# Kernel optimization log

Hardware: AMD Instinct MI355X
Metric: run time of the kernel (lower is better)

Reference implementation:

```python
import jax, jax.numpy as jnp
import numpy as np

V = 50257   # vocab_size
E = 512     # word_vec_size
H = 512     # hidden_size
L = 2       # num_layers
SOS = 1     # sos_id


def setup_inputs() -> dict:
    key = jax.random.key(0)
    ks = jax.random.split(key, 14)
    B, T, S = 32, 32, 128
    return {
        'tgt_seqs': jax.random.randint(ks[0], (B, T), 0, V),
        'decoder_hidden': jax.random.normal(ks[1], (L, B, H), jnp.float32) * 0.1,
        'encoder_outputs': jax.random.normal(ks[2], (S, B, H), jnp.float32),
        'attention_mask': jnp.zeros((B, S), dtype=bool),  # True = masked position
        'emb_W': jax.random.normal(ks[3], (V, E), jnp.float32) * 0.02,
        'gru_Wih': jax.random.normal(ks[4], (L, 3 * H, E), jnp.float32) * 0.02,
        'gru_Whh': jax.random.normal(ks[5], (L, 3 * H, H), jnp.float32) * 0.02,
        'gru_bih': jnp.zeros((L, 3 * H), jnp.float32),
        'gru_bhh': jnp.zeros((L, 3 * H), jnp.float32),
        'Wa': jax.random.normal(ks[6], (H, H), jnp.float32) * 0.02,
        'ba': jnp.zeros((H,), jnp.float32),
        'Wc': jax.random.normal(ks[7], (H, 2 * H), jnp.float32) * 0.02,
        'bc': jnp.zeros((H,), jnp.float32),
        'Ws': jax.random.normal(ks[8], (V, H), jnp.float32) * 0.02,
        'bs': jnp.zeros((V,), jnp.float32),
    }


def reference(tgt_seqs, decoder_hidden, encoder_outputs, attention_mask,
              emb_W, gru_Wih, gru_Whh, gru_bih, gru_bhh,
              Wa, ba, Wc, bc, Ws, bs):
    B, T = tgt_seqs.shape
    Hh = decoder_hidden.shape[-1]
    enc = jnp.transpose(encoder_outputs, (1, 0, 2))            # (B, S, H)
    enc_proj = jnp.einsum('bsh,gh->bsg', enc, Wa) + ba         # W_a(enc), precomputed
    # teacher-forced inputs: sos then shifted targets, time-major (T, B)
    tokens = jnp.concatenate(
        [jnp.full((B, 1), SOS, tgt_seqs.dtype), tgt_seqs[:, :-1]], axis=1).T

    def step(h, tok):
        x = emb_W[tok]                                          # (B, E)
        hs = []
        for l in range(L):                                      # small fixed layer loop
            gx = x @ gru_Wih[l].T + gru_bih[l]
            gh = h[l] @ gru_Whh[l].T + gru_bhh[l]
            r = jax.nn.sigmoid(gx[:, :Hh] + gh[:, :Hh])
            z = jax.nn.sigmoid(gx[:, Hh:2 * Hh] + gh[:, Hh:2 * Hh])
            n = jnp.tanh(gx[:, 2 * Hh:] + r * gh[:, 2 * Hh:])
            x = (1.0 - z) * n + z * h[l]
            hs.append(x)
        h_new = jnp.stack(hs)                                   # (L, B, H)
        # Luong general attention
        scores = jnp.einsum('bh,bsh->bs', x, enc_proj)          # (B, S)
        scores = jnp.where(attention_mask, -1e9, scores)
        attn = jax.nn.softmax(scores, axis=-1)
        ctx = jnp.einsum('bs,bsh->bh', attn, enc)               # (B, H)
        concat = jnp.tanh(jnp.concatenate([ctx, x], axis=-1) @ Wc.T + bc)
        return h_new, concat

    h_final, concats = jax.lax.scan(step, decoder_hidden, tokens)  # concats: (T, B, H)
    decoder_outputs = jnp.einsum('tbh,vh->tbv', concats, Ws) + bs  # (T, B, V)
    return decoder_outputs, h_final
```

## Files before the change

### kernel.cpp

```cpp
#include <hip/hip_runtime.h>
#include <hip/hip_bf16.h>
#include <stdint.h>
#include <stddef.h>

#define B_ 32
#define T_ 32
#define S_ 128
#define H_ 512
#define V_ 50257
#define VPAD 50304
#define TH3 1536

typedef __attribute__((ext_vector_type(8))) short short8x;
typedef __attribute__((ext_vector_type(4))) float f32x4;

__device__ __forceinline__ float sigf(float x) { return 1.f / (1.f + __expf(-x)); }
__device__ __forceinline__ float tanhfast(float x) {
  float e = __expf(2.f * x);
  return 1.f - 2.f / (e + 1.f);
}
__device__ __forceinline__ unsigned short f2bf(float x) {
  unsigned int u = __float_as_uint(x);
  return (unsigned short)((u + 0x7fffu + ((u >> 16) & 1u)) >> 16);
}
__device__ __forceinline__ float dot4(float4 a, float4 b) {
  return a.x * b.x + a.y * b.y + a.z * b.z + a.w * b.w;
}

__device__ __forceinline__ void async16(const unsigned short* g, short* l) {
  __builtin_amdgcn_global_load_lds(
      (const __attribute__((address_space(1))) unsigned int*)g,
      (__attribute__((address_space(3))) unsigned int*)l, 16, 0, 0);
}

__device__ __forceinline__ void store_wt(float* p, float v) {
  asm volatile("global_store_dword %0, %1, off sc0 sc1" :: "v"(p), "v"(v) : "memory");
}
__device__ __forceinline__ void store_wt4(float* p, f32x4 v) {
  asm volatile("global_store_dwordx4 %0, %1, off sc0 sc1" :: "v"(p), "v"(v) : "memory");
}

__device__ __forceinline__ void wait_flags(const int* flags, int n) {
  if (threadIdx.x < 64) {
    const int j = threadIdx.x;
    bool d0 = (j >= n), d1 = (j + 64 >= n);
    while (true) {
      if (!d0) d0 = __hip_atomic_load(flags + (size_t)j * 32, __ATOMIC_RELAXED,
                                      __HIP_MEMORY_SCOPE_SYSTEM) != 0;
      if (!d1) d1 = __hip_atomic_load(flags + (size_t)(j + 64) * 32, __ATOMIC_RELAXED,
                                      __HIP_MEMORY_SCOPE_SYSTEM) != 0;
      if (__all(d0 && d1)) break;
      __builtin_amdgcn_s_sleep(4);
    }
  }
  __syncthreads();
}

__device__ __forceinline__ void drain_and_flag(int* flag) {
  asm volatile("s_waitcnt vmcnt(0)" ::: "memory");
  __syncthreads();
  if (threadIdx.x == 0)
    __hip_atomic_store(flag, 1, __ATOMIC_RELAXED, __HIP_MEMORY_SCOPE_SYSTEM);
}

__global__ __launch_bounds__(256) void cvt_kernel(const float* __restrict__ Ws,
                                                  unsigned short* __restrict__ outb) {
  size_t i = ((size_t)blockIdx.x * 256 + threadIdx.x) * 4;
  if (i >= (size_t)VPAD * 512) return;
  float4 f;
  if (i < (size_t)V_ * 512) f = *(const float4*)(Ws + i);
  else f = make_float4(0.f, 0.f, 0.f, 0.f);
  ushort4 u;
  u.x = f2bf(f.x); u.y = f2bf(f.y); u.z = f2bf(f.z); u.w = f2bf(f.w);
  *(ushort4*)(outb + i) = u;
}

template <int MODE>
__global__ __launch_bounds__(256) void gemm_f32(const float* __restrict__ Asrc,
                                                const float* __restrict__ Bw,
                                                const float* __restrict__ bias,
                                                float* __restrict__ Cout,
                                                const int* __restrict__ tgt, int N) {
  __shared__ __align__(16) float As[16][68];
  __shared__ __align__(16) float Bs[16][68];
  const int tid = threadIdx.x;
  const int tx = tid & 15, ty = tid >> 4;
  const int m0 = blockIdx.y * 64, n0 = blockIdx.x * 64;
  const int srow = tid >> 2, skq = (tid & 3) * 4;
  const float* arow;
  {
    int m = m0 + srow;
    if (MODE == 0) {
      int t = m >> 5, b = m & 31;
      int tok = (t == 0) ? 1 : tgt[b * 32 + t - 1];
      arow = Asrc + (size_t)tok * 512;
    } else {
      int b = m >> 7, s = m & 127;
      arow = Asrc + ((size_t)s * 32 + b) * 512;
    }
  }
  const float* brow = Bw + (size_t)(n0 + srow) * 512;
  float acc[4][4] = {};
  for (int k0 = 0; k0 < 512; k0 += 16) {
    float4 av = *(const float4*)(arow + k0 + skq);
    float4 bv = *(const float4*)(brow + k0 + skq);
    __syncthreads();
    As[skq + 0][srow] = av.x; As[skq + 1][srow] = av.y;
    As[skq + 2][srow] = av.z; As[skq + 3][srow] = av.w;
    Bs[skq + 0][srow] = bv.x; Bs[skq + 1][srow] = bv.y;
    Bs[skq + 2][srow] = bv.z; Bs[skq + 3][srow] = bv.w;
    __syncthreads();
#pragma unroll
    for (int kk = 0; kk < 16; ++kk) {
      float4 a4 = *(const float4*)&As[kk][ty * 4];
      float4 b4 = *(const float4*)&Bs[kk][tx * 4];
      acc[0][0] += a4.x * b4.x; acc[0][1] += a4.x * b4.y; acc[0][2] += a4.x * b4.z; acc[0][3] += a4.x * b4.w;
      acc[1][0] += a4.y * b4.x; acc[1][1] += a4.y * b4.y; acc[1][2] += a4.y * b4.z; acc[1][3] += a4.y * b4.w;
      acc[2][0] += a4.z * b4.x; acc[2][1] += a4.z * b4.y; acc[2][2] += a4.z * b4.z; acc[2][3] += a4.z * b4.w;
      acc[3][0] += a4.w * b4.x; acc[3][1] += a4.w * b4.y; acc[3][2] += a4.w * b4.z; acc[3][3] += a4.w * b4.w;
    }
  }
  float4 b4 = *(const float4*)(bias + n0 + tx * 4);
#pragma unroll
  for (int i = 0; i < 4; ++i) {
    float4 o;
    o.x = acc[i][0] + b4.x; o.y = acc[i][1] + b4.y;
    o.z = acc[i][2] + b4.z; o.w = acc[i][3] + b4.w;
    *(float4*)(Cout + (size_t)(m0 + ty * 4 + i) * N + n0 + tx * 4) = o;
  }
}

__device__ __forceinline__ void cat_rows(int t, int gg, int b2, const float* wr,
                                         const float* __restrict__ ctxbuf,
                                         const float* __restrict__ x1buf,
                                         const float* __restrict__ bc,
                                         unsigned short* __restrict__ cbf) {
  const float* ctx = ctxbuf + (size_t)t * 16384 + b2 * 512;
  const float* x1c = x1buf + (size_t)t * 16384 + b2 * 512;
  float a = bc[gg];
#pragma unroll 4
  for (int k = 0; k < 512; k += 4) a += dot4(*(const float4*)(wr + k), *(const float4*)(ctx + k));
#pragma unroll 4
  for (int k = 0; k < 512; k += 4) a += dot4(*(const float4*)(wr + 512 + k), *(const float4*)(x1c + k));
  cbf[((size_t)t * 32 + b2) * 512 + gg] = f2bf(tanhfast(a));
}

__global__ __launch_bounds__(256) void seq_kernel(
    const float* __restrict__ dh, const float* __restrict__ enc,
    const unsigned char* __restrict__ mask,
    const float* __restrict__ Whh, const float* __restrict__ Wih,
    const float* __restrict__ bih, const float* __restrict__ bhh,
    const float* __restrict__ Wc, const float* __restrict__ bc,
    const float* __restrict__ gx0v, const float* __restrict__ encp,
    int* __restrict__ bar, float* __restrict__ x0buf, float* __restrict__ x1buf,
    float* __restrict__ attnbuf, float* __restrict__ ctxbuf,
    unsigned short* __restrict__ cbf, float* __restrict__ out_hf) {
  const int tid = threadIdx.x, bid = blockIdx.x;
  __shared__ __align__(16) float sm[3456];
  __shared__ __align__(16) float wlds[12288];
  const int lane = tid & 63, wv = tid >> 6;
  const int bb = lane & 31, rh = lane >> 5;

  int* fx0 = bar;
  int* fx1 = bar + 65536;
  int* fattn = bar + 196608;
  int* fctx = bar + 229376;

  if (bid < 64) {
    const int iset0 = bid * 8;
    for (int idx = tid; idx < 24 * 128; idx += 256) {
      const int rloc = idx >> 7, kq = (idx & 127) << 2;
      const int g = rloc >> 3, ii = rloc & 7;
      *(float4*)&wlds[rloc * 512 + kq] =
          *(const float4*)(Whh + (size_t)(g * 512 + iset0 + ii) * 512 + kq);
    }
  } else if (bid < 192) {
    const int iset0 = (bid - 64) * 4;
    for (int idx = tid; idx < 12 * 128; idx += 256) {
      const int rloc = idx >> 7, kq = (idx & 127) << 2;
      const int g = rloc >> 2, ii = rloc & 3;
      const size_t off = (size_t)(1536 + g * 512 + iset0 + ii) * 512 + kq;
      *(float4*)&wlds[rloc * 512 + kq] = *(const float4*)(Wih + off);
      *(float4*)&wlds[(12 + rloc) * 512 + kq] = *(const float4*)(Whh + off);
    }
  } else {
    const int gg0 = (bid < 224) ? (bid - 192) * 8 : 256 + (bid - 224) * 8;
    for (int idx = tid; idx < 8 * 256; idx += 256) {
      const int r = idx >> 8, kq = (idx & 255) << 2;
      *(float4*)&wlds[r * 1024 + kq] =
          *(const float4*)(Wc + (size_t)(gg0 + r) * 1024 + kq);
    }
  }
  __syncthreads();

  if (bid < 64) {
    const int iset0 = bid * 8;
    for (int t = 0; t < 32; ++t) {
      if (t > 0) wait_flags(fx0 + (size_t)(t - 1) * 2048, 64);
      const float* xsrc = (t == 0) ? dh : (x0buf + (size_t)(t - 1) * 16384);
      float acc[12];
#pragma unroll
      for (int r = 0; r < 12; ++r) acc[r] = 0.f;
      const float* xb = xsrc + bb * 512 + wv * 128;
      for (int c = 0; c < 4; ++c) {
        float4 xv[8];
#pragma unroll
        for (int u = 0; u < 8; ++u) xv[u] = *(const float4*)(xb + c * 32 + u * 4);
#pragma unroll
        for (int rr = 0; rr < 12; ++rr) {
          const int rloc = rh * 12 + rr;
          const float* wrow = wlds + (size_t)rloc * 512 + wv * 128 + c * 32;
#pragma unroll
          for (int u = 0; u < 8; ++u)
            acc[rr] += dot4(*(const float4*)(wrow + u * 4), xv[u]);
        }
      }
      __syncthreads();
#pragma unroll
      for (int rr = 0; rr < 12; ++rr)
        sm[wv * 768 + (rh * 12 + rr) * 32 + bb] = acc[rr];
      __syncthreads();
      {
        const int b2 = tid & 31, i2 = tid >> 5;
        const int ig = iset0 + i2;
        float s0 = bhh[ig], s1 = bhh[512 + ig], s2 = bhh[1024 + ig];
#pragma unroll
        for (int w = 0; w < 4; ++w) {
          s0 += sm[w * 768 + (i2) * 32 + b2];
          s1 += sm[w * 768 + (8 + i2) * 32 + b2];
          s2 += sm[w * 768 + (16 + i2) * 32 + b2];
        }
        const float* gx = gx0v + ((size_t)t * 32 + b2) * 1536;
        const float hv = xsrc[b2 * 512 + ig];
        const float r = sigf(gx[ig] + s0);
        const float z = sigf(gx[512 + ig] + s1);
        const float n = tanhfast(gx[1024 + ig] + r * s2);
        const float xn = (1.f - z) * n + z * hv;
        store_wt(x0buf + (size_t)t * 16384 + b2 * 512 + ig, xn);
        if (t == 31) out_hf[b2 * 512 + ig] = xn;
      }
      drain_and_flag(fx0 + ((size_t)t * 64 + bid) * 32);
    }
  } else if (bid < 192) {
    const int iset0 = (bid - 64) * 4;
    for (int t = 0; t < 32; ++t) {
      wait_flags(fx0 + (size_t)t * 2048, 64);
      if (t > 0) wait_flags(fx1 + (size_t)(t - 1) * 4096, 128);
      const float* xs0 = x0buf + (size_t)t * 16384;
      const float* xs1 = (t == 0) ? (dh + 16384) : (x1buf + (size_t)(t - 1) * 16384);
      float acc[12];
#pragma unroll
      for (int r = 0; r < 12; ++r) acc[r] = 0.f;
      {
        const float* xb = xs0 + bb * 512 + wv * 128;
        for (int c = 0; c < 4; ++c) {
          float4 xv[8];
#pragma unroll
          for (int u = 0; u < 8; ++u) xv[u] = *(const float4*)(xb + c * 32 + u * 4);
#pragma unroll
          for (int rr = 0; rr < 6; ++rr) {
            const int rloc = rh * 6 + rr;
            const float* wrow = wlds + (size_t)rloc * 512 + wv * 128 + c * 32;
#pragma unroll
            for (int u = 0; u < 8; ++u)
              acc[rr] += dot4(*(const float4*)(wrow + u * 4), xv[u]);
          }
        }
      }
      {
        const float* xb = xs1 + bb * 512 + wv * 128;
        for (int c = 0; c < 4; ++c) {
          float4 xv[8];
#pragma unroll
          for (int u = 0; u < 8; ++u) xv[u] = *(const float4*)(xb + c * 32 + u * 4);
#pragma unroll
          for (int rr = 0; rr < 6; ++rr) {
            const int rloc = rh * 6 + rr;
            const float* wrow = wlds + (size_t)(12 + rloc) * 512 + wv * 128 + c * 32;
#pragma unroll
            for (int u = 0; u < 8; ++u)
              acc[6 + rr] += dot4(*(const float4*)(wrow + u * 4), xv[u]);
          }
        }
      }
      __syncthreads();
#pragma unroll
      for (int rr = 0; rr < 6; ++rr) {
        sm[wv * 768 + (rh * 6 + rr) * 32 + bb] = acc[rr];
        sm[wv * 768 + (12 + rh * 6 + rr) * 32 + bb] = acc[6 + rr];
      }
      __syncthreads();
      if (tid < 128) {
        const int b2 = tid & 31, i2 = tid >> 5;
        const int ig = iset0 + i2;
        float gxs[3], ghs[3];
#pragma unroll
        for (int g = 0; g < 3; ++g) {
          float a = bih[1536 + g * 512 + ig];
          float h = bhh[1536 + g * 512 + ig];
#pragma unroll
          for (int w = 0; w < 4; ++w) {
            a += sm[w * 768 + (g * 4 + i2) * 32 + b2];
            h += sm[w * 768 + (12 + g * 4 + i2) * 32 + b2];
          }
          gxs[g] = a; ghs[g] = h;
        }
        const float hv = xs1[b2 * 512 + ig];
        const float r = sigf(gxs[0] + ghs[0]);
        const float z = sigf(gxs[1] + ghs[1]);
        const float n = tanhfast(gxs[2] + r * ghs[2]);
        const float xn = (1.f - z) * n + z * hv;
        store_wt(x1buf + (size_t)t * 16384 + b2 * 512 + ig, xn);
        if (t == 31) out_hf[16384 + b2 * 512 + ig] = xn;
      }
      drain_and_flag(fx1 + ((size_t)t * 128 + (bid - 64)) * 32);
    }
  } else if (bid < 224) {
    const int b = bid - 192;
    const float* wr = wlds + (size_t)(tid >> 5) * 1024;
    const int gg = b * 8 + (tid >> 5), b2 = tid & 31;
    for (int t = 0; t < 32; ++t) {
      wait_flags(fx1 + (size_t)t * 4096, 128);
      {
        const float* x1 = x1buf + (size_t)t * 16384 + b * 512;
        const int s = tid >> 1, kh = tid & 1;
        const float* ep = encp + ((size_t)b * 128 + s) * 512 + kh * 256;
        const float* xx = x1 + kh * 256;
        float a = 0.f;
#pragma unroll 8
        for (int k = 0; k < 256; k += 4)
          a += dot4(*(const float4*)(ep + k), *(const float4*)(xx + k));
        sm[tid] = a;
        __syncthreads();
        if (tid < 128) {
          float sc = sm[2 * tid] + sm[2 * tid + 1];
          if (mask[b * 128 + tid]) sc = -1e9f;
          sm[256 + tid] = sc;
        }
        __syncthreads();
        if (tid < 64) {
          float m1 = fmaxf(sm[256 + tid], sm[256 + tid + 64]);
#pragma unroll
          for (int off = 32; off; off >>= 1) m1 = fmaxf(m1, __shfl_xor(m1, off));
          float e0 = __expf(sm[256 + tid] - m1), e1 = __expf(sm[256 + tid + 64] - m1);
          float ssum = e0 + e1;
#pragma unroll
          for (int off = 32; off; off >>= 1) ssum += __shfl_xor(ssum, off);
          float inv = 1.f / ssum;
          sm[384 + tid] = e0 * inv;
          sm[384 + tid + 64] = e1 * inv;
        }
        __syncthreads();
        if (tid < 128) store_wt(attnbuf + (size_t)t * 4096 + b * 128 + tid, sm[384 + tid]);
      }
      drain_and_flag(fattn + ((size_t)t * 32 + b) * 32);
      if (t > 0) {
        wait_flags(fctx + (size_t)(t - 1) * 1024, 32);
        cat_rows(t - 1, gg, b2, wr, ctxbuf, x1buf, bc, cbf);
      }
    }
    wait_flags(fctx + (size_t)31 * 1024, 32);
    cat_rows(31, gg, b2, wr, ctxbuf, x1buf, bc, cbf);
  } else {
    const int b = bid - 224;
    const float* wr = wlds + (size_t)(tid >> 5) * 1024;
    const int gg = 256 + b * 8 + (tid >> 5), b2 = tid & 31;
    for (int t = 0; t < 32; ++t) {
      wait_flags(fattn + ((size_t)t * 32 + b) * 32, 1);
      if (tid < 128) sm[tid] = attnbuf[(size_t)t * 4096 + b * 128 + tid];
      __syncthreads();
      if (tid < 128) {
        const int h4 = tid * 4;
        float4 c = make_float4(0.f, 0.f, 0.f, 0.f);
#pragma unroll 8
        for (int s = 0; s < 128; ++s) {
          const float a = sm[s];
          const float4 e = *(const float4*)(enc + ((size_t)s * 32 + b) * 512 + h4);
          c.x += a * e.x; c.y += a * e.y; c.z += a * e.z; c.w += a * e.w;
        }
        f32x4 cc = {c.x, c.y, c.z, c.w};
        store_wt4(ctxbuf + (size_t)t * 16384 + b * 512 + h4, cc);
      }
      drain_and_flag(fctx + ((size_t)t * 32 + b) * 32);
      if (t > 0) {
        wait_flags(fx1 + (size_t)(t - 1) * 4096, 128);
        wait_flags(fctx + (size_t)(t - 1) * 1024, 32);
        cat_rows(t - 1, gg, b2, wr, ctxbuf, x1buf, bc, cbf);
      }
    }
    wait_flags(fx1 + (size_t)31 * 4096, 128);
    wait_flags(fctx + (size_t)31 * 1024, 32);
    cat_rows(31, gg, b2, wr, ctxbuf, x1buf, bc, cbf);
  }
}

__global__ __launch_bounds__(256) void proj_kernel(const unsigned short* __restrict__ A,
                                                   const unsigned short* __restrict__ Bw,
                                                   const float* __restrict__ bs,
                                                   float* __restrict__ C) {
  __shared__ short8x AsV[512];
  __shared__ short8x BsV[512];
  short* As = (short*)AsV;
  short* Bs = (short*)BsV;
  const int tid = threadIdx.x;
  const int lane = tid & 63, wv = tid >> 6;
  const int m0 = blockIdx.x * 128;
  const int n0 = blockIdx.y * 128;
  const int wm = (wv >> 1) * 64, wn = (wv & 1) * 64;
  f32x4 acc[4][4] = {};
  const int sr = lane >> 2, sb = (lane & 3) * 8;
  const unsigned short* gA1 = A + (size_t)(m0 + wv * 16 + sr) * 512 + sb;
  const unsigned short* gA2 = gA1 + (size_t)64 * 512;
  const unsigned short* gB1 = Bw + (size_t)(n0 + wv * 16 + sr) * 512 + sb;
  const unsigned short* gB2 = gB1 + (size_t)64 * 512;
  short* lA1 = As + (wv * 16) * 32;
  short* lA2 = As + (64 + wv * 16) * 32;
  short* lB1 = Bs + (wv * 16) * 32;
  short* lB2 = Bs + (64 + wv * 16) * 32;
  const int rA = wm + (lane & 15);
  const int rB = wn + (lane & 15);
  const int kb = (lane >> 4) * 8;
  for (int kt = 0; kt < 16; ++kt) {
    const int ko = kt * 32;
    __syncthreads();
    async16(gA1 + ko, lA1);
    async16(gA2 + ko, lA2);
    async16(gB1 + ko, lB1);
    async16(gB2 + ko, lB2);
    __syncthreads();
    short8x af[4], bf[4];
#pragma unroll
    for (int i = 0; i < 4; ++i) af[i] = *(const short8x*)(As + (rA + i * 16) * 32 + kb);
#pragma unroll
    for (int i = 0; i < 4; ++i) bf[i] = *(const short8x*)(Bs + (rB + i * 16) * 32 + kb);
#pragma unroll
    for (int mo = 0; mo < 4; ++mo)
#pragma unroll
      for (int no = 0; no < 4; ++no)
        acc[mo][no] = __builtin_amdgcn_mfma_f32_16x16x32_bf16(af[mo], bf[no], acc[mo][no], 0, 0, 0);
  }
#pragma unroll
  for (int no = 0; no < 4; ++no) {
    const int col = n0 + wn + no * 16 + (lane & 15);
    if (col < V_) {
      const float bsv = bs[col];
#pragma unroll
      for (int mo = 0; mo < 4; ++mo) {
        const int row = m0 + wm + mo * 16 + ((lane >> 4) << 2);
        f32x4 v = acc[mo][no];
        C[(size_t)(row + 0) * V_ + col] = v[0] + bsv;
        C[(size_t)(row + 1) * V_ + col] = v[1] + bsv;
        C[(size_t)(row + 2) * V_ + col] = v[2] + bsv;
        C[(size_t)(row + 3) * V_ + col] = v[3] + bsv;
      }
    }
  }
}

extern "C" void kernel_launch(void* const* d_in, const int* in_sizes, int n_in,
                              void* d_out, int out_size, void* d_ws, size_t ws_size,
                              hipStream_t stream) {
  (void)in_sizes; (void)n_in; (void)out_size; (void)ws_size;
  const int* tgt = (const int*)d_in[0];
  const float* dh = (const float*)d_in[1];
  const float* enc = (const float*)d_in[2];
  const unsigned char* mask = (const unsigned char*)d_in[3];
  const float* embW = (const float*)d_in[4];
  const float* Wih = (const float*)d_in[5];
  const float* Whh = (const float*)d_in[6];
  const float* bih = (const float*)d_in[7];
  const float* bhh = (const float*)d_in[8];
  const float* Wa = (const float*)d_in[9];
  const float* ba = (const float*)d_in[10];
  const float* Wc = (const float*)d_in[11];
  const float* bc = (const float*)d_in[12];
  const float* Ws = (const float*)d_in[13];
  const float* bs = (const float*)d_in[14];
  float* out = (float*)d_out;

  char* w = (char*)d_ws;
  int* bar = (int*)w;
  float* x0buf = (float*)(w + (1 << 20));
  float* x1buf = x0buf + 524288;
  float* attnbuf = x1buf + 524288;
  float* ctxbuf = attnbuf + 131072;
  float* gx0v = ctxbuf + 524288;
  float* encp = gx0v + 1572864;
  unsigned short* cbf = (unsigned short*)(encp + 2097152);
  unsigned short* wsb = cbf + 524288;

  hipMemsetAsync(bar, 0, 1 << 20, stream);
  cvt_kernel<<<25152, 256, 0, stream>>>(Ws, wsb);
  gemm_f32<0><<<dim3(24, 16), 256, 0, stream>>>(embW, Wih, bih, gx0v, tgt, 1536);
  gemm_f32<1><<<dim3(8, 64), 256, 0, stream>>>(enc, Wa, ba, encp, nullptr, 512);
  seq_kernel<<<256, 256, 0, stream>>>(dh, enc, mask, Whh, Wih, bih, bhh, Wc, bc,
                                      gx0v, encp, bar, x0buf, x1buf, attnbuf, ctxbuf,
                                      cbf, out + (size_t)1024 * V_);
  proj_kernel<<<dim3(8, 393), 256, 0, stream>>>(cbf, wsb, bs, out);
}
```

Before: 1.898 ms.

## Replace flag barriers with sentinel polling on data buffers in recurrent kernel

Removes the separate flag array and drain-then-flag handshake. Instead, data buffers are pre-filled with a 0xFFFFFFFF NaN sentinel and consumers poll the actual data until no sentinel remains. This removes one store round-trip and the vmcnt drain on each producer step, shortening the critical path of the sequential GRU/attention chain. The cost is that consumers must poll larger buffers, memset traffic grows, and correctness depends on no legitimate value matching the sentinel bit pattern and on 16-byte stores being observed atomically.

```diff
diff --git a/kernel.cpp b/kernel.cpp
--- a/kernel.cpp
+++ b/kernel.cpp
@@ -40,27 +40,44 @@
   asm volatile("global_store_dwordx4 %0, %1, off sc0 sc1" :: "v"(p), "v"(v) : "memory");
 }
 
-__device__ __forceinline__ void wait_flags(const int* flags, int n) {
-  if (threadIdx.x < 64) {
-    const int j = threadIdx.x;
-    bool d0 = (j >= n), d1 = (j + 64 >= n);
+__device__ __forceinline__ int f4ok(f32x4 v) {
+  return (__float_as_uint(v[0]) != 0xFFFFFFFFu) &
+         (__float_as_uint(v[1]) != 0xFFFFFFFFu) &
+         (__float_as_uint(v[2]) != 0xFFFFFFFFu) &
+         (__float_as_uint(v[3]) != 0xFFFFFFFFu);
+}
+
+__device__ __forceinline__ void poll16k(const float* buf) {
+  const float* p = buf + threadIdx.x * 4;
+  while (true) {
+    f32x4 a, b, c, d;
+    asm volatile(
+        "global_load_dwordx4 %0, %4, off sc0 sc1\n\t"
+        "global_load_dwordx4 %1, %5, off sc0 sc1\n\t"
+        "global_load_dwordx4 %2, %6, off sc0 sc1\n\t"
+        "global_load_dwordx4 %3, %7, off sc0 sc1\n\t"
+        "s_waitcnt vmcnt(0)"
+        : "=v"(a), "=v"(b), "=v"(c), "=v"(d)
+        : "v"(p), "v"(p + 1024), "v"(p + 2048), "v"(p + 3072)
+        : "memory");
+    if (f4ok(a) & f4ok(b) & f4ok(c) & f4ok(d)) break;
+    __builtin_amdgcn_s_sleep(1);
+  }
+  __syncthreads();
+}
+
+__device__ __forceinline__ void poll_small(const float* buf, int n) {
+  if ((int)threadIdx.x < n) {
+    const float* p = buf + threadIdx.x * 4;
     while (true) {
-      if (!d0) d0 = __hip_atomic_load(flags + (size_t)j * 32, __ATOMIC_RELAXED,
-                                      __HIP_MEMORY_SCOPE_SYSTEM) != 0;
-      if (!d1) d1 = __hip_atomic_load(flags + (size_t)(j + 64) * 32, __ATOMIC_RELAXED,
-                                      __HIP_MEMORY_SCOPE_SYSTEM) != 0;
-      if (__all(d0 && d1)) break;
-      __builtin_amdgcn_s_sleep(4);
+      f32x4 a;
+      asm volatile("global_load_dwordx4 %0, %1, off sc0 sc1\n\ts_waitcnt vmcnt(0)"
+                   : "=v"(a) : "v"(p) : "memory");
+      if (f4ok(a)) break;
+      __builtin_amdgcn_s_sleep(1);
     }
   }
   __syncthreads();
-}
-
-__device__ __forceinline__ void drain_and_flag(int* flag) {
-  asm volatile("s_waitcnt vmcnt(0)" ::: "memory");
-  __syncthreads();
-  if (threadIdx.x == 0)
-    __hip_atomic_store(flag, 1, __ATOMIC_RELAXED, __HIP_MEMORY_SCOPE_SYSTEM);
 }
 
 __global__ __launch_bounds__(256) void cvt_kernel(const float* __restrict__ Ws,
@@ -152,7 +169,7 @@
     const float* __restrict__ bih, const float* __restrict__ bhh,
     const float* __restrict__ Wc, const float* __restrict__ bc,
     const float* __restrict__ gx0v, const float* __restrict__ encp,
-    int* __restrict__ bar, float* __restrict__ x0buf, float* __restrict__ x1buf,
+    float* __restrict__ x0buf, float* __restrict__ x1buf,
     float* __restrict__ attnbuf, float* __restrict__ ctxbuf,
     unsigned short* __restrict__ cbf, float* __restrict__ out_hf) {
   const int tid = threadIdx.x, bid = blockIdx.x;
@@ -160,11 +177,6 @@
   __shared__ __align__(16) float wlds[12288];
   const int lane = tid & 63, wv = tid >> 6;
   const int bb = lane & 31, rh = lane >> 5;
-
-  int* fx0 = bar;
-  int* fx1 = bar + 65536;
-  int* fattn = bar + 196608;
-  int* fctx = bar + 229376;
 
   if (bid < 64) {
     const int iset0 = bid * 8;
@@ -196,7 +208,7 @@
   if (bid < 64) {
     const int iset0 = bid * 8;
     for (int t = 0; t < 32; ++t) {
-      if (t > 0) wait_flags(fx0 + (size_t)(t - 1) * 2048, 64);
+      if (t > 0) poll16k(x0buf + (size_t)(t - 1) * 16384);
       const float* xsrc = (t == 0) ? dh : (x0buf + (size_t)(t - 1) * 16384);
       float acc[12];
 #pragma unroll
@@ -239,15 +251,13 @@
         store_wt(x0buf + (size_t)t * 16384 + b2 * 512 + ig, xn);
         if (t == 31) out_hf[b2 * 512 + ig] = xn;
       }
-      drain_and_flag(fx0 + ((size_t)t * 64 + bid) * 32);
+      __syncthreads();
     }
   } else if (bid < 192) {
     const int iset0 = (bid - 64) * 4;
     for (int t = 0; t < 32; ++t) {
-      wait_flags(fx0 + (size_t)t * 2048, 64);
-      if (t > 0) wait_flags(fx1 + (size_t)(t - 1) * 4096, 128);
       const float* xs0 = x0buf + (size_t)t * 16384;
-      const float* xs1 = (t == 0) ? (dh + 16384) : (x1buf + (size_t)(t - 1) * 16384);
+      poll16k(xs0);
       float acc[12];
 #pragma unroll
       for (int r = 0; r < 12; ++r) acc[r] = 0.f;
@@ -267,6 +277,8 @@
           }
         }
       }
+      const float* xs1 = (t == 0) ? (dh + 16384) : (x1buf + (size_t)(t - 1) * 16384);
+      if (t > 0) poll16k(xs1);
       {
         const float* xb = xs1 + bb * 512 + wv * 128;
         for (int c = 0; c < 4; ++c) {
@@ -313,14 +325,14 @@
         store_wt(x1buf + (size_t)t * 16384 + b2 * 512 + ig, xn);
         if (t == 31) out_hf[16384 + b2 * 512 + ig] = xn;
       }
-      drain_and_flag(fx1 + ((size_t)t * 128 + (bid - 64)) * 32);
+      __syncthreads();
     }
   } else if (bid < 224) {
     const int b = bid - 192;
     const float* wr = wlds + (size_t)(tid >> 5) * 1024;
     const int gg = b * 8 + (tid >> 5), b2 = tid & 31;
     for (int t = 0; t < 32; ++t) {
-      wait_flags(fx1 + (size_t)t * 4096, 128);
+      poll_small(x1buf + (size_t)t * 16384 + b * 512, 128);
       {
         const float* x1 = x1buf + (size_t)t * 16384 + b * 512;
         const int s = tid >> 1, kh = tid & 1;
@@ -352,21 +364,23 @@
         }
         __syncthreads();
         if (tid < 128) store_wt(attnbuf + (size_t)t * 4096 + b * 128 + tid, sm[384 + tid]);
-      }
-      drain_and_flag(fattn + ((size_t)t * 32 + b) * 32);
+        __syncthreads();
+      }
       if (t > 0) {
-        wait_flags(fctx + (size_t)(t - 1) * 1024, 32);
+        poll16k(ctxbuf + (size_t)(t - 1) * 16384);
+        poll16k(x1buf + (size_t)(t - 1) * 16384);
         cat_rows(t - 1, gg, b2, wr, ctxbuf, x1buf, bc, cbf);
       }
     }
-    wait_flags(fctx + (size_t)31 * 1024, 32);
+    poll16k(ctxbuf + (size_t)31 * 16384);
+    poll16k(x1buf + (size_t)31 * 16384);
     cat_rows(31, gg, b2, wr, ctxbuf, x1buf, bc, cbf);
   } else {
     const int b = bid - 224;
     const float* wr = wlds + (size_t)(tid >> 5) * 1024;
     const int gg = 256 + b * 8 + (tid >> 5), b2 = tid & 31;
     for (int t = 0; t < 32; ++t) {
-      wait_flags(fattn + ((size_t)t * 32 + b) * 32, 1);
+      poll_small(attnbuf + (size_t)t * 4096 + b * 128, 32);
       if (tid < 128) sm[tid] = attnbuf[(size_t)t * 4096 + b * 128 + tid];
       __syncthreads();
       if (tid < 128) {
@@ -381,15 +395,15 @@
         f32x4 cc = {c.x, c.y, c.z, c.w};
         store_wt4(ctxbuf + (size_t)t * 16384 + b * 512 + h4, cc);
       }
-      drain_and_flag(fctx + ((size_t)t * 32 + b) * 32);
+      __syncthreads();
       if (t > 0) {
-        wait_flags(fx1 + (size_t)(t - 1) * 4096, 128);
-        wait_flags(fctx + (size_t)(t - 1) * 1024, 32);
+        poll16k(x1buf + (size_t)(t - 1) * 16384);
+        poll16k(ctxbuf + (size_t)(t - 1) * 16384);
         cat_rows(t - 1, gg, b2, wr, ctxbuf, x1buf, bc, cbf);
       }
     }
-    wait_flags(fx1 + (size_t)31 * 4096, 128);
-    wait_flags(fctx + (size_t)31 * 1024, 32);
+    poll16k(x1buf + (size_t)31 * 16384);
+    poll16k(ctxbuf + (size_t)31 * 16384);
     cat_rows(31, gg, b2, wr, ctxbuf, x1buf, bc, cbf);
   }
 }
@@ -479,8 +493,7 @@
   float* out = (float*)d_out;
 
   char* w = (char*)d_ws;
-  int* bar = (int*)w;
-  float* x0buf = (float*)(w + (1 << 20));
+  float* x0buf = (float*)w;
   float* x1buf = x0buf + 524288;
   float* attnbuf = x1buf + 524288;
   float* ctxbuf = attnbuf + 131072;
@@ -489,12 +502,12 @@
   unsigned short* cbf = (unsigned short*)(encp + 2097152);
   unsigned short* wsb = cbf + 524288;
 
-  hipMemsetAsync(bar, 0, 1 << 20, stream);
+  hipMemsetAsync(w, 0xFF, 6815744, stream);
   cvt_kernel<<<25152, 256, 0, stream>>>(Ws, wsb);
   gemm_f32<0><<<dim3(24, 16), 256, 0, stream>>>(embW, Wih, bih, gx0v, tgt, 1536);
   gemm_f32<1><<<dim3(8, 64), 256, 0, stream>>>(enc, Wa, ba, encp, nullptr, 512);
   seq_kernel<<<256, 256, 0, stream>>>(dh, enc, mask, Whh, Wih, bih, bhh, Wc, bc,
-                                      gx0v, encp, bar, x0buf, x1buf, attnbuf, ctxbuf,
+                                      gx0v, encp, x0buf, x1buf, attnbuf, ctxbuf,
                                       cbf, out + (size_t)1024 * V_);
   proj_kernel<<<dim3(8, 393), 256, 0, stream>>>(cbf, wsb, bs, out);
 }
```

After: 2.438 ms. 1.28x slower.
